# Optimization experiments

Measured on AMD Instinct MI355X. Metric: run time of the kernel, lower is better.

Reference implementation:

```python
import jax, jax.numpy as jnp
import numpy as np

# Hard-coded model hyperparams (RuntimeParams)
B, L, H, NH, FF, DEPTH = 256, 256, 128, 8, 512, 4
PEAK, NCAT, CVOC, KMAX, NNUM, NDIM, TSLOT = 500000, 8, 50001, 8, 4, 32, 256
SCALE = (H // NH) ** -0.5


def _ln(x, g, b):
    m = x.mean(-1, keepdims=True)
    v = ((x - m) ** 2).mean(-1, keepdims=True)
    return (x - m) / jnp.sqrt(v + 1e-5) * g + b


def _block(x, mask, p):
    ln1_g, ln1_b, qw, qb, ow, ob, w1, b1, w2, b2, ln2_g, ln2_b = p
    b, n, c = x.shape
    src = _ln(x, ln1_g, ln1_b)
    qkv = (src @ qw + qb).reshape(b, n, 3, NH, c // NH).transpose(2, 0, 3, 1, 4)
    q, k, v = qkv[0], qkv[1], qkv[2]  # [b, nh, n, dh]
    dots = jnp.einsum('bhid,bhjd->bhij', q, k) * SCALE
    dots = jnp.where(mask[:, None, None, :], dots, -jnp.inf)
    attn = jax.nn.softmax(dots, axis=-1)
    out = jnp.einsum('bhij,bhjd->bhid', attn, v).transpose(0, 2, 1, 3).reshape(b, n, c)
    x = x + out @ ow + ob
    h = _ln(x, ln2_g, ln2_b)
    h = jax.nn.gelu(h @ w1 + b1, approximate=False) @ w2 + b2
    return x + h


def _encode(cat_vals, cat_lens, num_arr, cat_tables, num_W):
    # Vectorized form of the per-sample _encode_fields python loop:
    # per categorical field: mean of embeddings over the ragged value list
    # per numeric field: bias-free linear projection; then mean over all fields.
    emb = cat_tables[jnp.arange(NCAT)[None, :, None], cat_vals]  # [B,F,K,H]
    pos = (jnp.arange(KMAX)[None, None, :] < cat_lens[:, :, None]).astype(emb.dtype)
    fc = (emb * pos[..., None]).sum(2) / cat_lens[:, :, None].astype(emb.dtype)  # [B,F,H]
    fn = jnp.einsum('bfd,fdh->bfh', num_arr, num_W)  # [B,Fn,H]
    return (fc.sum(1) + fn.sum(1)) / (NCAT + NNUM)  # mean over all fields


def setup_inputs() -> dict:
    key = jax.random.key(0)
    ks = iter(jax.random.split(key, 40))
    nk = lambda: next(ks)
    d = {}
    d['item_seq'] = jax.random.randint(nk(), (B, L), 0, PEAK + 5)
    d['action_seq'] = jax.random.randint(nk(), (B, L), 0, 5)
    d['time_diff'] = jax.random.randint(nk(), (B, L), 0, TSLOT)
    seq_lens = jax.random.randint(nk(), (B,), L // 2, L + 1)
    d['mask'] = jnp.arange(L)[None, :] < seq_lens[:, None]
    for pre in ('u', 'i'):
        vals = jax.random.randint(nk(), (B, NCAT, KMAX), 1, CVOC)
        lens = jax.random.randint(nk(), (B, NCAT), 1, KMAX + 1)
        vals = jnp.where(jnp.arange(KMAX)[None, None, :] < lens[:, :, None], vals, 0)
        d[pre + '_cat_vals'] = vals
        d[pre + '_cat_lens'] = lens
        d[pre + '_num'] = jax.random.normal(nk(), (B, NNUM, NDIM), dtype=jnp.float32)
    s = 0.02
    d['item_table'] = (jax.random.normal(nk(), (PEAK + 5, H), dtype=jnp.float32) * s).at[0].set(0.0)
    d['act_table'] = jax.random.normal(nk(), (5, H), dtype=jnp.float32) * s
    d['time_table'] = jax.random.normal(nk(), (TSLOT, H), dtype=jnp.float32) * s
    d['cat_tables'] = (jax.random.normal(nk(), (NCAT, CVOC, H), dtype=jnp.float32) * s).at[:, 0, :].set(0.0)
    d['num_W'] = jax.random.normal(nk(), (NNUM, NDIM, H), dtype=jnp.float32) * s
    d['global_token'] = jax.random.normal(nk(), (1, 1, H), dtype=jnp.float32)
    d['ln1_g'] = jnp.ones((DEPTH, H)); d['ln1_b'] = jnp.zeros((DEPTH, H))
    d['qkv_w'] = jax.random.normal(nk(), (DEPTH, H, 3 * H), dtype=jnp.float32) * s
    d['qkv_b'] = jnp.zeros((DEPTH, 3 * H))
    d['out_w'] = jax.random.normal(nk(), (DEPTH, H, H), dtype=jnp.float32) * s
    d['out_b'] = jnp.zeros((DEPTH, H))
    d['mlp_w1'] = jax.random.normal(nk(), (DEPTH, H, FF), dtype=jnp.float32) * s
    d['mlp_b1'] = jnp.zeros((DEPTH, FF))
    d['mlp_w2'] = jax.random.normal(nk(), (DEPTH, FF, H), dtype=jnp.float32) * s
    d['mlp_b2'] = jnp.zeros((DEPTH, H))
    d['ln2_g'] = jnp.ones((DEPTH, H)); d['ln2_b'] = jnp.zeros((DEPTH, H))
    d['bott_w'] = jax.random.normal(nk(), (H, H), dtype=jnp.float32) * s
    d['bott_b'] = jnp.zeros((H,))
    d['cls_w'] = jax.random.normal(nk(), (H, 1), dtype=jnp.float32) * s
    d['cls_b'] = jnp.zeros((1,))
    return d


def reference(item_seq, action_seq, time_diff, mask, u_cat_vals, u_cat_lens, u_num,
              i_cat_vals, i_cat_lens, i_num, item_table, act_table, time_table,
              cat_tables, num_W, global_token, ln1_g, ln1_b, qkv_w, qkv_b,
              out_w, out_b, mlp_w1, mlp_b1, mlp_w2, mlp_b2, ln2_g, ln2_b,
              bott_w, bott_b, cls_w, cls_b):
    b = item_seq.shape[0]
    seq_feat = item_table[item_seq] + act_table[action_seq] + time_table[time_diff]  # [B,L,H]
    u = _encode(u_cat_vals, u_cat_lens, u_num, cat_tables, num_W)[:, None, :]
    i = _encode(i_cat_vals, i_cat_lens, i_num, cat_tables, num_W)[:, None, :]
    cls = jnp.broadcast_to(global_token, (b, 1, H))
    x = jnp.concatenate([cls, u, i, seq_feat], axis=1)  # [B, 3+L, H]
    fmask = jnp.concatenate([jnp.ones((b, 3), dtype=bool), mask], axis=1)
    for dd in range(DEPTH):
        p = (ln1_g[dd], ln1_b[dd], qkv_w[dd], qkv_b[dd], out_w[dd], out_b[dd],
             mlp_w1[dd], mlp_b1[dd], mlp_w2[dd], mlp_b2[dd], ln2_g[dd], ln2_b[dd])
        x = _block(x, fmask, p)
    latent = x[:, 0, :]
    logits = (jax.nn.relu(latent @ bott_w + bott_b) @ cls_w + cls_b)[:, 0]
    embed = latent / jnp.maximum(jnp.linalg.norm(latent, axis=-1, keepdims=True), 1e-12)
    return logits, embed
```

## Files before the change

### kernel.cpp

```cpp
#include <hip/hip_runtime.h>
#include <cstdio>

#define BATCH 256
#define SEQL 256
#define NPOS 259
#define TTOK (BATCH*NPOS)
#define HD 128
#define NHEAD 8
#define FF 512
#define DEPTH 4
#define CVOC 50001

typedef unsigned short u16;
typedef unsigned int u32;
typedef __bf16 bf16x8 __attribute__((ext_vector_type(8)));
typedef float f32x4 __attribute__((ext_vector_type(4)));
typedef float f32x16 __attribute__((ext_vector_type(16)));

typedef const __attribute__((address_space(1))) u32 gas_u32;
typedef __attribute__((address_space(3))) u32 las_u32;
#define GLOAD16(gptr, lptr) \
  __builtin_amdgcn_global_load_lds((gas_u32*)(gptr), (las_u32*)(lptr), 16, 0, 0)

__device__ __forceinline__ u16 f2bf(float f) {
  u32 i = __float_as_uint(f);
  u32 r = (i + 0x7FFFu + ((i >> 16) & 1u)) >> 16;
  return (u16)r;
}

__global__ void k_transpose(const float* __restrict__ in, u16* __restrict__ out,
                            int D, int K, int N) {
  int idx = blockIdx.x * 256 + threadIdx.x;
  int total = D * K * N;
  if (idx >= total) return;
  int k = idx % K; int rem = idx / K; int n = rem % N; int d = rem / N;
  out[idx] = f2bf(in[(d * K + k) * N + n]);
}

__global__ __launch_bounds__(128)
void k_build(const int* __restrict__ item_seq, const int* __restrict__ act_seq,
             const int* __restrict__ tdiff,
             const int* __restrict__ ucv, const int* __restrict__ ucl, const float* __restrict__ unum,
             const int* __restrict__ icv, const int* __restrict__ icl, const float* __restrict__ inum,
             const float* __restrict__ item_t, const float* __restrict__ act_t,
             const float* __restrict__ time_t, const float* __restrict__ cat_t,
             const float* __restrict__ numW, const float* __restrict__ gtok,
             float* __restrict__ x) {
  int pos = blockIdx.x, b = blockIdx.y, h = threadIdx.x;
  float v;
  if (pos == 0) {
    v = gtok[h];
  } else if (pos <= 2) {
    const int* cv = (pos == 1) ? ucv : icv;
    const int* cl = (pos == 1) ? ucl : icl;
    const float* nm = (pos == 1) ? unum : inum;
    float acc = 0.f;
    for (int f = 0; f < 8; ++f) {
      float s = 0.f;
      for (int k = 0; k < 8; ++k) {
        int idx = cv[(b * 8 + f) * 8 + k];
        s += cat_t[((size_t)f * CVOC + idx) * HD + h];
      }
      acc += s / (float)cl[b * 8 + f];
    }
    for (int f = 0; f < 4; ++f)
      for (int d = 0; d < 32; ++d)
        acc += nm[(b * 4 + f) * 32 + d] * numW[(f * 32 + d) * HD + h];
    v = acc * (1.f / 12.f);
  } else {
    int l = pos - 3;
    v = item_t[(size_t)item_seq[b * SEQL + l] * HD + h]
      + act_t[(size_t)act_seq[b * SEQL + l] * HD + h]
      + time_t[(size_t)tdiff[b * SEQL + l] * HD + h];
  }
  x[((size_t)b * NPOS + pos) * HD + h] = v;
}

__global__ __launch_bounds__(256)
void k_ln(const float* __restrict__ x, const float* __restrict__ g,
          const float* __restrict__ be, u16* __restrict__ out) {
  int t = blockIdx.x * 4 + (threadIdx.x >> 6);
  int lane = threadIdx.x & 63;
  const float* xr = x + (size_t)t * HD;
  float a = xr[lane], c = xr[lane + 64];
  float s = a + c, s2 = a * a + c * c;
  #pragma unroll
  for (int o = 32; o; o >>= 1) { s += __shfl_xor(s, o); s2 += __shfl_xor(s2, o); }
  float mean = s * (1.f / HD);
  float var = s2 * (1.f / HD) - mean * mean;
  float rstd = rsqrtf(var + 1e-5f);
  out[(size_t)t * HD + lane]      = f2bf((a - mean) * rstd * g[lane] + be[lane]);
  out[(size_t)t * HD + lane + 64] = f2bf((c - mean) * rstd * g[lane + 64] + be[lane + 64]);
}

template <int ACT, bool QS>
__global__ __launch_bounds__(256)
void k_gemm(const u16* __restrict__ X, const u16* __restrict__ WT,
            const float* __restrict__ bias, u16* __restrict__ outp,
            int K, int N) {
  __shared__ __align__(16) u16 lA[128 * 32];
  __shared__ __align__(16) u16 lB[128 * 32];
  const int tid = threadIdx.x;
  const int wave = tid >> 6, lane = tid & 63;
  const int row0 = blockIdx.x * 128;
  const int n0 = blockIdx.y * 128;
  const int wr = (wave >> 1) * 64, wc = (wave & 1) * 64;
  const int sr = lane >> 2;
  const int sc = ((lane & 3) ^ ((lane >> 3) & 3)) << 3;
  const u16* gA0 = X  + (size_t)(row0 + wave * 16 + sr) * K + sc;
  const u16* gA1 = X  + (size_t)(row0 + 64 + wave * 16 + sr) * K + sc;
  const u16* gB0 = WT + (size_t)(n0 + wave * 16 + sr) * K + sc;
  const u16* gB1 = WT + (size_t)(n0 + 64 + wave * 16 + sr) * K + sc;
  u16* lA0 = &lA[wave * 512];
  u16* lA1 = &lA[2048 + wave * 512];
  u16* lB0 = &lB[wave * 512];
  u16* lB1 = &lB[2048 + wave * 512];
  const int q = lane & 15;
  const int cg = lane >> 4;
  const int rdoff = ((cg ^ ((q >> 1) & 3)) << 3);
  f32x4 acc[4][4] = {};
  for (int k0 = 0; k0 < K; k0 += 32) {
    __syncthreads();
    GLOAD16(gA0 + k0, lA0);
    GLOAD16(gA1 + k0, lA1);
    GLOAD16(gB0 + k0, lB0);
    GLOAD16(gB1 + k0, lB1);
    __syncthreads();
    bf16x8 af[4], bf[4];
    #pragma unroll
    for (int i = 0; i < 4; ++i)
      af[i] = *(const bf16x8*)&lA[(wr + i * 16 + q) * 32 + rdoff];
    #pragma unroll
    for (int j = 0; j < 4; ++j)
      bf[j] = *(const bf16x8*)&lB[(wc + j * 16 + q) * 32 + rdoff];
    #pragma unroll
    for (int i = 0; i < 4; ++i)
      #pragma unroll
      for (int j = 0; j < 4; ++j)
        acc[i][j] = __builtin_amdgcn_mfma_f32_16x16x32_bf16(af[i], bf[j], acc[i][j], 0, 0, 0);
  }
  const int rg4 = cg * 4;
  #pragma unroll
  for (int i = 0; i < 4; ++i) {
    #pragma unroll
    for (int j = 0; j < 4; ++j) {
      int col = n0 + wc + j * 16 + q;
      float bv = bias[col];
      float scl = (QS && col < 128) ? 0.25f : 1.f;
      #pragma unroll
      for (int jj = 0; jj < 4; ++jj) {
        int row = row0 + wr + i * 16 + rg4 + jj;
        float v = acc[i][j][jj] + bv;
        if (ACT == 1) v = 0.5f * v * (1.f + erff(v * 0.70710678118654752f));
        if (QS) v *= scl;
        outp[(size_t)row * N + col] = f2bf(v);
      }
    }
  }
}

__global__ __launch_bounds__(256)
void k_gemm_ln(const u16* __restrict__ X, const u16* __restrict__ WT,
               const float* __restrict__ bias, float* __restrict__ xio,
               const float* __restrict__ g, const float* __restrict__ be,
               u16* __restrict__ srcout, int K) {
  __shared__ __align__(16) u16 lA[128 * 32];
  __shared__ __align__(16) u16 lB[128 * 32];
  __shared__ float part[128][2][2];
  const int tid = threadIdx.x;
  const int wave = tid >> 6, lane = tid & 63;
  const int row0 = blockIdx.x * 128;
  const int wr = (wave >> 1) * 64, wc = (wave & 1) * 64;
  const int whalf = wave & 1;
  const int sr = lane >> 2;
  const int sc = ((lane & 3) ^ ((lane >> 3) & 3)) << 3;
  const u16* gA0 = X  + (size_t)(row0 + wave * 16 + sr) * K + sc;
  const u16* gA1 = X  + (size_t)(row0 + 64 + wave * 16 + sr) * K + sc;
  const u16* gB0 = WT + (size_t)(wave * 16 + sr) * K + sc;
  const u16* gB1 = WT + (size_t)(64 + wave * 16 + sr) * K + sc;
  u16* lA0 = &lA[wave * 512];
  u16* lA1 = &lA[2048 + wave * 512];
  u16* lB0 = &lB[wave * 512];
  u16* lB1 = &lB[2048 + wave * 512];
  const int q = lane & 15;
  const int cg = lane >> 4;
  const int rdoff = ((cg ^ ((q >> 1) & 3)) << 3);
  f32x4 acc[4][4] = {};
  for (int k0 = 0; k0 < K; k0 += 32) {
    __syncthreads();
    GLOAD16(gA0 + k0, lA0);
    GLOAD16(gA1 + k0, lA1);
    GLOAD16(gB0 + k0, lB0);
    GLOAD16(gB1 + k0, lB1);
    __syncthreads();
    bf16x8 af[4], bf[4];
    #pragma unroll
    for (int i = 0; i < 4; ++i)
      af[i] = *(const bf16x8*)&lA[(wr + i * 16 + q) * 32 + rdoff];
    #pragma unroll
    for (int j = 0; j < 4; ++j)
      bf[j] = *(const bf16x8*)&lB[(wc + j * 16 + q) * 32 + rdoff];
    #pragma unroll
    for (int i = 0; i < 4; ++i)
      #pragma unroll
      for (int j = 0; j < 4; ++j)
        acc[i][j] = __builtin_amdgcn_mfma_f32_16x16x32_bf16(af[i], bf[j], acc[i][j], 0, 0, 0);
  }
  const int rg4 = cg * 4;
  float ps[4][4], ps2[4][4];
  #pragma unroll
  for (int i = 0; i < 4; ++i)
    #pragma unroll
    for (int jj = 0; jj < 4; ++jj) { ps[i][jj] = 0.f; ps2[i][jj] = 0.f; }
  #pragma unroll
  for (int i = 0; i < 4; ++i) {
    #pragma unroll
    for (int j = 0; j < 4; ++j) {
      int col = wc + j * 16 + q;
      float bv = bias[col];
      #pragma unroll
      for (int jj = 0; jj < 4; ++jj) {
        int row = row0 + wr + i * 16 + rg4 + jj;
        float xv = xio[(size_t)row * 128 + col] + acc[i][j][jj] + bv;
        acc[i][j][jj] = xv;
        ps[i][jj] += xv;
        ps2[i][jj] += xv * xv;
      }
    }
  }
  #pragma unroll
  for (int o = 1; o < 16; o <<= 1) {
    #pragma unroll
    for (int i = 0; i < 4; ++i)
      #pragma unroll
      for (int jj = 0; jj < 4; ++jj) {
        ps[i][jj]  += __shfl_xor(ps[i][jj], o);
        ps2[i][jj] += __shfl_xor(ps2[i][jj], o);
      }
  }
  if (q == 0) {
    #pragma unroll
    for (int i = 0; i < 4; ++i)
      #pragma unroll
      for (int jj = 0; jj < 4; ++jj) {
        int rl = wr + i * 16 + rg4 + jj;
        part[rl][whalf][0] = ps[i][jj];
        part[rl][whalf][1] = ps2[i][jj];
      }
  }
  __syncthreads();
  #pragma unroll
  for (int i = 0; i < 4; ++i) {
    #pragma unroll
    for (int jj = 0; jj < 4; ++jj) {
      int rl = wr + i * 16 + rg4 + jj;
      float S  = part[rl][0][0] + part[rl][1][0];
      float S2 = part[rl][0][1] + part[rl][1][1];
      float mean = S * (1.f / 128.f);
      float rstd = rsqrtf(S2 * (1.f / 128.f) - mean * mean + 1e-5f);
      int row = row0 + rl;
      #pragma unroll
      for (int j = 0; j < 4; ++j) {
        int col = wc + j * 16 + q;
        float xv = acc[i][j][jj];
        xio[(size_t)row * 128 + col] = xv;
        srcout[(size_t)row * 128 + col] = f2bf((xv - mean) * rstd * g[col] + be[col]);
      }
    }
  }
}

#define VSTR2 296
__global__ __launch_bounds__(256)
void k_attn(const u16* __restrict__ qkv, const int* __restrict__ mask,
            u16* __restrict__ out) {
  int h = blockIdx.x, b = blockIdx.y;
  __shared__ __align__(16) u16 Klin[9 * 512];
  __shared__ __align__(16) u16 Vt[16 * VSTR2];
  __shared__ int part[4];
  const int tid = threadIdx.x;
  int mv = (mask[b * SEQL + tid] != 0) ? 1 : 0;
  #pragma unroll
  for (int o = 32; o; o >>= 1) mv += __shfl_xor(mv, o);
  if ((tid & 63) == 0) part[tid >> 6] = mv;
  for (int idx = tid; idx < 576; idx += 256) {
    int r = idx >> 1, h2 = idx & 1;
    uint4 val = make_uint4(0, 0, 0, 0);
    if (r < NPOS)
      val = *(const uint4*)&qkv[((size_t)(b * NPOS + r)) * 384 + h * 16 + 128 + h2 * 8];
    *(uint4*)&Klin[(r >> 5) * 512 + h2 * 256 + (r & 31) * 8] = val;
  }
  for (int r = tid; r < 288; r += 256) {
    u16 tmp[16];
    if (r < NPOS) {
      const u16* vp = &qkv[((size_t)(b * NPOS + r)) * 384 + h * 16 + 256];
      *(uint4*)&tmp[0] = *(const uint4*)&vp[0];
      *(uint4*)&tmp[8] = *(const uint4*)&vp[8];
    } else {
      #pragma unroll
      for (int d = 0; d < 16; ++d) tmp[d] = 0;
    }
    #pragma unroll
    for (int d = 0; d < 16; ++d) Vt[d * VSTR2 + r] = tmp[d];
  }
  __syncthreads();
  const int nvalid = part[0] + part[1] + part[2] + part[3] + 3;
  const int ktiles = (nvalid + 31) >> 5;
  const int wave = tid >> 6, lane = tid & 63;
  const int q5 = lane & 31, hi = lane >> 5;
  const f32x16 zf = {};
  for (int qt = wave; qt < 9; qt += 4) {
    int qrow = qt * 32 + q5;
    int qr = (qrow < NPOS) ? qrow : (NPOS - 1);
    bf16x8 qf = *(const bf16x8*)&qkv[((size_t)(b * NPOS + qr)) * 384 + h * 16 + hi * 8];
    float m = -1e30f, l = 0.f;
    f32x16 acc = {};
    for (int kt = 0; kt < ktiles; ++kt) {
      bf16x8 kf = *(const bf16x8*)&Klin[kt * 512 + lane * 8];
      f32x16 s4 = __builtin_amdgcn_mfma_f32_32x32x16_bf16(kf, qf, zf, 0, 0, 0);
      float p[16];
      float tmax = -1e30f;
      #pragma unroll
      for (int r = 0; r < 16; ++r) {
        int kr = kt * 32 + (r & 3) + 8 * (r >> 2) + 4 * hi;
        float v = (kr < nvalid) ? s4[r] : -1e30f;
        p[r] = v;
        tmax = fmaxf(tmax, v);
      }
      tmax = fmaxf(tmax, __shfl_xor(tmax, 32));
      float mnew = fmaxf(m, tmax);
      float fac = __expf(m - mnew);
      float tsum = 0.f;
      #pragma unroll
      for (int r = 0; r < 16; ++r) { p[r] = __expf(p[r] - mnew); tsum += p[r]; }
      tsum += __shfl_xor(tsum, 32);
      l = l * fac + tsum;
      m = mnew;
      #pragma unroll
      for (int r = 0; r < 8; ++r) acc[r] *= fac;
      u32 w[8], xw[8];
      #pragma unroll
      for (int i = 0; i < 8; ++i)
        asm("v_cvt_pk_bf16_f32 %0, %1, %2" : "=v"(w[i]) : "v"(p[2 * i]), "v"(p[2 * i + 1]));
      #pragma unroll
      for (int i = 0; i < 8; ++i) xw[i] = (u32)__shfl_xor((int)w[i], 32);
      union { u32 u[4]; bf16x8 v; } f1, f2;
      if (hi) {
        f1.u[0] = xw[2]; f1.u[1] = xw[3]; f1.u[2] = w[2]; f1.u[3] = w[3];
        f2.u[0] = xw[6]; f2.u[1] = xw[7]; f2.u[2] = w[6]; f2.u[3] = w[7];
      } else {
        f1.u[0] = w[0]; f1.u[1] = w[1]; f1.u[2] = xw[0]; f1.u[3] = xw[1];
        f2.u[0] = w[4]; f2.u[1] = w[5]; f2.u[2] = xw[4]; f2.u[3] = xw[5];
      }
      bf16x8 vf0 = {}, vf1 = {};
      if (q5 < 16) {
        vf0 = *(const bf16x8*)&Vt[q5 * VSTR2 + kt * 32 + hi * 8];
        vf1 = *(const bf16x8*)&Vt[q5 * VSTR2 + kt * 32 + 16 + hi * 8];
      }
      acc = __builtin_amdgcn_mfma_f32_32x32x16_bf16(vf0, f1.v, acc, 0, 0, 0);
      acc = __builtin_amdgcn_mfma_f32_32x32x16_bf16(vf1, f2.v, acc, 0, 0, 0);
    }
    if (qrow < NPOS) {
      float linv = 1.f / l;
      u16* op = &out[((size_t)(b * NPOS + qrow)) * HD + h * 16];
      u32 w0 = (u32)f2bf(acc[0] * linv) | ((u32)f2bf(acc[1] * linv) << 16);
      u32 w1 = (u32)f2bf(acc[2] * linv) | ((u32)f2bf(acc[3] * linv) << 16);
      u32 w2 = (u32)f2bf(acc[4] * linv) | ((u32)f2bf(acc[5] * linv) << 16);
      u32 w3 = (u32)f2bf(acc[6] * linv) | ((u32)f2bf(acc[7] * linv) << 16);
      *(uint2*)&op[4 * hi] = make_uint2(w0, w1);
      *(uint2*)&op[8 + 4 * hi] = make_uint2(w2, w3);
    }
  }
}

__global__ __launch_bounds__(128)
void k_head(const float* __restrict__ x, const float* __restrict__ bw,
            const float* __restrict__ bb, const float* __restrict__ cw,
             const float* __restrict__ cb, float* __restrict__ dout) {
  int b = blockIdx.x, n = threadIdx.x;
  __shared__ float lat[HD];
  __shared__ float redp[2], redss[2];
  float lv = x[((size_t)b * NPOS) * HD + n];
  lat[n] = lv;
  __syncthreads();
  float t = 0.f;
  for (int k = 0; k < HD; ++k) t += lat[k] * bw[k * HD + n];
  t += bb[n];
  t = fmaxf(t, 0.f);
  float p = t * cw[n];
  float ss = lv * lv;
  #pragma unroll
  for (int o = 32; o; o >>= 1) { p += __shfl_xor(p, o); ss += __shfl_xor(ss, o); }
  if ((n & 63) == 0) { redp[n >> 6] = p; redss[n >> 6] = ss; }
  __syncthreads();
  float psum = redp[0] + redp[1];
  float ssum = redss[0] + redss[1];
  if (n == 0) dout[b] = psum + cb[0];
  float nrm = fmaxf(sqrtf(ssum), 1e-12f);
  dout[256 + (size_t)b * HD + n] = lv / nrm;
}

extern "C" void kernel_launch(void* const* d_in, const int* in_sizes, int n_in,
                              void* d_out, int out_size, void* d_ws, size_t ws_size,
                              hipStream_t stream) {
  const int* item_seq = (const int*)d_in[0];
  const int* action_seq = (const int*)d_in[1];
  const int* time_diff = (const int*)d_in[2];
  const int* mask = (const int*)d_in[3];
  const int* u_cv = (const int*)d_in[4];
  const int* u_cl = (const int*)d_in[5];
  const float* u_num = (const float*)d_in[6];
  const int* i_cv = (const int*)d_in[7];
  const int* i_cl = (const int*)d_in[8];
  const float* i_num = (const float*)d_in[9];
  const float* item_t = (const float*)d_in[10];
  const float* act_t = (const float*)d_in[11];
  const float* time_t = (const float*)d_in[12];
  const float* cat_t = (const float*)d_in[13];
  const float* num_W = (const float*)d_in[14];
  const float* gtok = (const float*)d_in[15];
  const float* ln1_g = (const float*)d_in[16];
  const float* ln1_b = (const float*)d_in[17];
  const float* qkv_w = (const float*)d_in[18];
  const float* qkv_b = (const float*)d_in[19];
  const float* out_w = (const float*)d_in[20];
  const float* out_b = (const float*)d_in[21];
  const float* w1 = (const float*)d_in[22];
  const float* b1 = (const float*)d_in[23];
  const float* w2 = (const float*)d_in[24];
  const float* b2 = (const float*)d_in[25];
  const float* ln2_g = (const float*)d_in[26];
  const float* ln2_b = (const float*)d_in[27];
  const float* bott_w = (const float*)d_in[28];
  const float* bott_b = (const float*)d_in[29];
  const float* cls_w = (const float*)d_in[30];
  const float* cls_b = (const float*)d_in[31];

  const size_t off_x   = 0;
  const size_t off_src = 33947648;
  const size_t off_big = 50921472;
  const size_t off_wT  = 118816768;
  const size_t need    = 120389632;
  if (ws_size < need) {
    fprintf(stderr, "kernel_launch: ws_size %zu < needed %zu\n", ws_size, need);
    return;
  }
  char* ws = (char*)d_ws;
  float* x   = (float*)(ws + off_x);
  u16* src   = (u16*)(ws + off_src);
  u16* big   = (u16*)(ws + off_big);
  u16* wT    = (u16*)(ws + off_wT);
  u16* qkvT  = wT;
  u16* outT  = wT + 196608;
  u16* w1T   = wT + 262144;
  u16* w2T   = wT + 524288;

  k_transpose<<<(4 * 128 * 384 + 255) / 256, 256, 0, stream>>>(qkv_w, qkvT, 4, 128, 384);
  k_transpose<<<(4 * 128 * 128 + 255) / 256, 256, 0, stream>>>(out_w, outT, 4, 128, 128);
  k_transpose<<<(4 * 128 * 512 + 255) / 256, 256, 0, stream>>>(w1, w1T, 4, 128, 512);
  k_transpose<<<(4 * 512 * 128 + 255) / 256, 256, 0, stream>>>(w2, w2T, 4, 512, 128);

  k_build<<<dim3(NPOS, BATCH), 128, 0, stream>>>(
      item_seq, action_seq, time_diff, u_cv, u_cl, u_num, i_cv, i_cl, i_num,
      item_t, act_t, time_t, cat_t, num_W, gtok, x);

  k_ln<<<TTOK / 4, 256, 0, stream>>>(x, ln1_g, ln1_b, src);

  const int rt = TTOK / 128;
  for (int dd = 0; dd < DEPTH; ++dd) {
    k_gemm<0, true><<<dim3(rt, 3), 256, 0, stream>>>(
        src, qkvT + dd * 49152, qkv_b + dd * 384, big, 128, 384);
    k_attn<<<dim3(NHEAD, BATCH), 256, 0, stream>>>(big, mask, src);
    k_gemm_ln<<<dim3(rt, 1), 256, 0, stream>>>(
        src, outT + dd * 16384, out_b + dd * HD, x,
        ln2_g + dd * HD, ln2_b + dd * HD, src, 128);
    k_gemm<1, false><<<dim3(rt, 4), 256, 0, stream>>>(
        src, w1T + dd * 65536, b1 + dd * FF, big, 128, 512);
    const float* ng = (dd < 3) ? (ln1_g + (dd + 1) * HD) : (ln1_g + dd * HD);
    const float* nb = (dd < 3) ? (ln1_b + (dd + 1) * HD) : (ln1_b + dd * HD);
    k_gemm_ln<<<dim3(rt, 1), 256, 0, stream>>>(
        big, w2T + dd * 65536, b2 + dd * HD, x, ng, nb, src, 512);
  }

  k_head<<<BATCH, 128, 0, stream>>>(x, bott_w, bott_b, cls_w, cls_b, (float*)d_out);
}
```

Before: 840.9 us.

## Fuse weight transposes and initial LN, widen attention blocks to one wave per query tile

Merges the four weight-transpose launches into one kernel and folds the first LayerNorm into the embedding build kernel, so fewer launches run and the x buffer is not re-read. The attention kernel now runs 576 threads, nine waves with one 32-row query tile each, instead of four waves looping over tiles. It also uses exp2 with the log2e factor folded into the Q scale, and raises wave priority around the MFMA calls. Larger blocks may lower occupancy or raise register pressure in the attention kernel.

```diff
diff --git a/kernel.cpp b/kernel.cpp
--- a/kernel.cpp
+++ b/kernel.cpp
@@ -22,19 +22,26 @@
 #define GLOAD16(gptr, lptr) \
   __builtin_amdgcn_global_load_lds((gas_u32*)(gptr), (las_u32*)(lptr), 16, 0, 0)
 
+#define QSCALE 0.36067376022224085f
+
 __device__ __forceinline__ u16 f2bf(float f) {
   u32 i = __float_as_uint(f);
   u32 r = (i + 0x7FFFu + ((i >> 16) & 1u)) >> 16;
   return (u16)r;
 }
 
-__global__ void k_transpose(const float* __restrict__ in, u16* __restrict__ out,
-                            int D, int K, int N) {
+__global__ void k_transpose_all(const float* __restrict__ qkv_w, const float* __restrict__ out_w,
+                                const float* __restrict__ w1, const float* __restrict__ w2,
+                                u16* __restrict__ wT) {
   int idx = blockIdx.x * 256 + threadIdx.x;
-  int total = D * K * N;
-  if (idx >= total) return;
-  int k = idx % K; int rem = idx / K; int n = rem % N; int d = rem / N;
-  out[idx] = f2bf(in[(d * K + k) * N + n]);
+  const float* in; int K, N, local;
+  if (idx < 196608)      { in = qkv_w; K = 128; N = 384; local = idx; }
+  else if (idx < 262144) { in = out_w; K = 128; N = 128; local = idx - 196608; }
+  else if (idx < 524288) { in = w1;    K = 128; N = 512; local = idx - 262144; }
+  else if (idx < 786432) { in = w2;    K = 512; N = 128; local = idx - 524288; }
+  else return;
+  int k = local % K; int rem = local / K; int n = rem % N; int d = rem / N;
+  wT[idx] = f2bf(in[(d * K + k) * N + n]);
 }
 
 __global__ __launch_bounds__(128)
@@ -45,7 +52,8 @@
              const float* __restrict__ item_t, const float* __restrict__ act_t,
              const float* __restrict__ time_t, const float* __restrict__ cat_t,
              const float* __restrict__ numW, const float* __restrict__ gtok,
-             float* __restrict__ x) {
+             const float* __restrict__ g, const float* __restrict__ be,
+             float* __restrict__ x, u16* __restrict__ src) {
   int pos = blockIdx.x, b = blockIdx.y, h = threadIdx.x;
   float v;
   if (pos == 0) {
@@ -73,24 +81,18 @@
       + act_t[(size_t)act_seq[b * SEQL + l] * HD + h]
       + time_t[(size_t)tdiff[b * SEQL + l] * HD + h];
   }
-  x[((size_t)b * NPOS + pos) * HD + h] = v;
-}
-
-__global__ __launch_bounds__(256)
-void k_ln(const float* __restrict__ x, const float* __restrict__ g,
-          const float* __restrict__ be, u16* __restrict__ out) {
-  int t = blockIdx.x * 4 + (threadIdx.x >> 6);
-  int lane = threadIdx.x & 63;
-  const float* xr = x + (size_t)t * HD;
-  float a = xr[lane], c = xr[lane + 64];
-  float s = a + c, s2 = a * a + c * c;
+  size_t t = (size_t)b * NPOS + pos;
+  x[t * HD + h] = v;
+  __shared__ float red[2][2];
+  float s = v, s2 = v * v;
   #pragma unroll
   for (int o = 32; o; o >>= 1) { s += __shfl_xor(s, o); s2 += __shfl_xor(s2, o); }
-  float mean = s * (1.f / HD);
-  float var = s2 * (1.f / HD) - mean * mean;
-  float rstd = rsqrtf(var + 1e-5f);
-  out[(size_t)t * HD + lane]      = f2bf((a - mean) * rstd * g[lane] + be[lane]);
-  out[(size_t)t * HD + lane + 64] = f2bf((c - mean) * rstd * g[lane + 64] + be[lane + 64]);
+  if ((h & 63) == 0) { red[h >> 6][0] = s; red[h >> 6][1] = s2; }
+  __syncthreads();
+  float S = red[0][0] + red[1][0], S2 = red[0][1] + red[1][1];
+  float mean = S * (1.f / HD);
+  float rstd = rsqrtf(S2 * (1.f / HD) - mean * mean + 1e-5f);
+  src[t * HD + h] = f2bf((v - mean) * rstd * g[h] + be[h]);
 }
 
 template <int ACT, bool QS>
@@ -146,7 +148,7 @@
     for (int j = 0; j < 4; ++j) {
       int col = n0 + wc + j * 16 + q;
       float bv = bias[col];
-      float scl = (QS && col < 128) ? 0.25f : 1.f;
+      float scl = (QS && col < 128) ? QSCALE : 1.f;
       #pragma unroll
       for (int jj = 0; jj < 4; ++jj) {
         int row = row0 + wr + i * 16 + rg4 + jj;
@@ -271,7 +273,7 @@
 }
 
 #define VSTR2 296
-__global__ __launch_bounds__(256)
+__global__ __launch_bounds__(576)
 void k_attn(const u16* __restrict__ qkv, const int* __restrict__ mask,
             u16* __restrict__ out) {
   int h = blockIdx.x, b = blockIdx.y;
@@ -279,18 +281,21 @@
   __shared__ __align__(16) u16 Vt[16 * VSTR2];
   __shared__ int part[4];
   const int tid = threadIdx.x;
-  int mv = (mask[b * SEQL + tid] != 0) ? 1 : 0;
-  #pragma unroll
-  for (int o = 32; o; o >>= 1) mv += __shfl_xor(mv, o);
-  if ((tid & 63) == 0) part[tid >> 6] = mv;
-  for (int idx = tid; idx < 576; idx += 256) {
-    int r = idx >> 1, h2 = idx & 1;
+  if (tid < 256) {
+    int mv = (mask[b * SEQL + tid] != 0) ? 1 : 0;
+    #pragma unroll
+    for (int o = 32; o; o >>= 1) mv += __shfl_xor(mv, o);
+    if ((tid & 63) == 0) part[tid >> 6] = mv;
+  }
+  {
+    int r = tid >> 1, h2 = tid & 1;
     uint4 val = make_uint4(0, 0, 0, 0);
     if (r < NPOS)
       val = *(const uint4*)&qkv[((size_t)(b * NPOS + r)) * 384 + h * 16 + 128 + h2 * 8];
     *(uint4*)&Klin[(r >> 5) * 512 + h2 * 256 + (r & 31) * 8] = val;
   }
-  for (int r = tid; r < 288; r += 256) {
+  if (tid < 288) {
+    int r = tid;
     u16 tmp[16];
     if (r < NPOS) {
       const u16* vp = &qkv[((size_t)(b * NPOS + r)) * 384 + h * 16 + 256];
@@ -309,74 +314,77 @@
   const int wave = tid >> 6, lane = tid & 63;
   const int q5 = lane & 31, hi = lane >> 5;
   const f32x16 zf = {};
-  for (int qt = wave; qt < 9; qt += 4) {
-    int qrow = qt * 32 + q5;
-    int qr = (qrow < NPOS) ? qrow : (NPOS - 1);
-    bf16x8 qf = *(const bf16x8*)&qkv[((size_t)(b * NPOS + qr)) * 384 + h * 16 + hi * 8];
-    float m = -1e30f, l = 0.f;
-    f32x16 acc = {};
-    for (int kt = 0; kt < ktiles; ++kt) {
-      bf16x8 kf = *(const bf16x8*)&Klin[kt * 512 + lane * 8];
-      f32x16 s4 = __builtin_amdgcn_mfma_f32_32x32x16_bf16(kf, qf, zf, 0, 0, 0);
-      float p[16];
-      float tmax = -1e30f;
-      #pragma unroll
-      for (int r = 0; r < 16; ++r) {
-        int kr = kt * 32 + (r & 3) + 8 * (r >> 2) + 4 * hi;
-        float v = (kr < nvalid) ? s4[r] : -1e30f;
-        p[r] = v;
-        tmax = fmaxf(tmax, v);
-      }
-      tmax = fmaxf(tmax, __shfl_xor(tmax, 32));
-      float mnew = fmaxf(m, tmax);
-      float fac = __expf(m - mnew);
-      float tsum = 0.f;
-      #pragma unroll
-      for (int r = 0; r < 16; ++r) { p[r] = __expf(p[r] - mnew); tsum += p[r]; }
-      tsum += __shfl_xor(tsum, 32);
-      l = l * fac + tsum;
-      m = mnew;
-      #pragma unroll
-      for (int r = 0; r < 8; ++r) acc[r] *= fac;
-      u32 w[8], xw[8];
-      #pragma unroll
-      for (int i = 0; i < 8; ++i)
-        asm("v_cvt_pk_bf16_f32 %0, %1, %2" : "=v"(w[i]) : "v"(p[2 * i]), "v"(p[2 * i + 1]));
-      #pragma unroll
-      for (int i = 0; i < 8; ++i) xw[i] = (u32)__shfl_xor((int)w[i], 32);
-      union { u32 u[4]; bf16x8 v; } f1, f2;
-      if (hi) {
-        f1.u[0] = xw[2]; f1.u[1] = xw[3]; f1.u[2] = w[2]; f1.u[3] = w[3];
-        f2.u[0] = xw[6]; f2.u[1] = xw[7]; f2.u[2] = w[6]; f2.u[3] = w[7];
-      } else {
-        f1.u[0] = w[0]; f1.u[1] = w[1]; f1.u[2] = xw[0]; f1.u[3] = xw[1];
-        f2.u[0] = w[4]; f2.u[1] = w[5]; f2.u[2] = xw[4]; f2.u[3] = xw[5];
-      }
-      bf16x8 vf0 = {}, vf1 = {};
-      if (q5 < 16) {
-        vf0 = *(const bf16x8*)&Vt[q5 * VSTR2 + kt * 32 + hi * 8];
-        vf1 = *(const bf16x8*)&Vt[q5 * VSTR2 + kt * 32 + 16 + hi * 8];
-      }
-      acc = __builtin_amdgcn_mfma_f32_32x32x16_bf16(vf0, f1.v, acc, 0, 0, 0);
-      acc = __builtin_amdgcn_mfma_f32_32x32x16_bf16(vf1, f2.v, acc, 0, 0, 0);
-    }
-    if (qrow < NPOS) {
-      float linv = 1.f / l;
-      u16* op = &out[((size_t)(b * NPOS + qrow)) * HD + h * 16];
-      u32 w0 = (u32)f2bf(acc[0] * linv) | ((u32)f2bf(acc[1] * linv) << 16);
-      u32 w1 = (u32)f2bf(acc[2] * linv) | ((u32)f2bf(acc[3] * linv) << 16);
-      u32 w2 = (u32)f2bf(acc[4] * linv) | ((u32)f2bf(acc[5] * linv) << 16);
-      u32 w3 = (u32)f2bf(acc[6] * linv) | ((u32)f2bf(acc[7] * linv) << 16);
-      *(uint2*)&op[4 * hi] = make_uint2(w0, w1);
-      *(uint2*)&op[8 + 4 * hi] = make_uint2(w2, w3);
-    }
+  const int qt = wave;
+  int qrow = qt * 32 + q5;
+  int qr = (qrow < NPOS) ? qrow : (NPOS - 1);
+  bf16x8 qf = *(const bf16x8*)&qkv[((size_t)(b * NPOS + qr)) * 384 + h * 16 + hi * 8];
+  float m = -1e30f, l = 0.f;
+  f32x16 acc = {};
+  for (int kt = 0; kt < ktiles; ++kt) {
+    bf16x8 kf = *(const bf16x8*)&Klin[kt * 512 + lane * 8];
+    __builtin_amdgcn_s_setprio(1);
+    f32x16 s4 = __builtin_amdgcn_mfma_f32_32x32x16_bf16(kf, qf, zf, 0, 0, 0);
+    __builtin_amdgcn_s_setprio(0);
+    float p[16];
+    float tmax = -1e30f;
+    #pragma unroll
+    for (int r = 0; r < 16; ++r) {
+      int kr = kt * 32 + (r & 3) + 8 * (r >> 2) + 4 * hi;
+      float v = (kr < nvalid) ? s4[r] : -1e30f;
+      p[r] = v;
+      tmax = fmaxf(tmax, v);
+    }
+    tmax = fmaxf(tmax, __shfl_xor(tmax, 32));
+    float mnew = fmaxf(m, tmax);
+    float fac = exp2f(m - mnew);
+    float tsum = 0.f;
+    #pragma unroll
+    for (int r = 0; r < 16; ++r) { p[r] = exp2f(p[r] - mnew); tsum += p[r]; }
+    tsum += __shfl_xor(tsum, 32);
+    l = l * fac + tsum;
+    m = mnew;
+    #pragma unroll
+    for (int r = 0; r < 8; ++r) acc[r] *= fac;
+    u32 w[8], xw[8];
+    #pragma unroll
+    for (int i = 0; i < 8; ++i)
+      asm("v_cvt_pk_bf16_f32 %0, %1, %2" : "=v"(w[i]) : "v"(p[2 * i]), "v"(p[2 * i + 1]));
+    #pragma unroll
+    for (int i = 0; i < 8; ++i) xw[i] = (u32)__shfl_xor((int)w[i], 32);
+    union { u32 u[4]; bf16x8 v; } f1, f2;
+    if (hi) {
+      f1.u[0] = xw[2]; f1.u[1] = xw[3]; f1.u[2] = w[2]; f1.u[3] = w[3];
+      f2.u[0] = xw[6]; f2.u[1] = xw[7]; f2.u[2] = w[6]; f2.u[3] = w[7];
+    } else {
+      f1.u[0] = w[0]; f1.u[1] = w[1]; f1.u[2] = xw[0]; f1.u[3] = xw[1];
+      f2.u[0] = w[4]; f2.u[1] = w[5]; f2.u[2] = xw[4]; f2.u[3] = xw[5];
+    }
+    bf16x8 vf0 = {}, vf1 = {};
+    if (q5 < 16) {
+      vf0 = *(const bf16x8*)&Vt[q5 * VSTR2 + kt * 32 + hi * 8];
+      vf1 = *(const bf16x8*)&Vt[q5 * VSTR2 + kt * 32 + 16 + hi * 8];
+    }
+    __builtin_amdgcn_s_setprio(1);
+    acc = __builtin_amdgcn_mfma_f32_32x32x16_bf16(vf0, f1.v, acc, 0, 0, 0);
+    acc = __builtin_amdgcn_mfma_f32_32x32x16_bf16(vf1, f2.v, acc, 0, 0, 0);
+    __builtin_amdgcn_s_setprio(0);
+  }
+  if (qrow < NPOS) {
+    float linv = 1.f / l;
+    u16* op = &out[((size_t)(b * NPOS + qrow)) * HD + h * 16];
+    u32 w0 = (u32)f2bf(acc[0] * linv) | ((u32)f2bf(acc[1] * linv) << 16);
+    u32 w1 = (u32)f2bf(acc[2] * linv) | ((u32)f2bf(acc[3] * linv) << 16);
+    u32 w2 = (u32)f2bf(acc[4] * linv) | ((u32)f2bf(acc[5] * linv) << 16);
+    u32 w3 = (u32)f2bf(acc[6] * linv) | ((u32)f2bf(acc[7] * linv) << 16);
+    *(uint2*)&op[4 * hi] = make_uint2(w0, w1);
+    *(uint2*)&op[8 + 4 * hi] = make_uint2(w2, w3);
   }
 }
 
 __global__ __launch_bounds__(128)
 void k_head(const float* __restrict__ x, const float* __restrict__ bw,
             const float* __restrict__ bb, const float* __restrict__ cw,
-             const float* __restrict__ cb, float* __restrict__ dout) {
+            const float* __restrict__ cb, float* __restrict__ dout) {
   int b = blockIdx.x, n = threadIdx.x;
   __shared__ float lat[HD];
   __shared__ float redp[2], redss[2];
@@ -455,22 +463,17 @@
   u16* w1T   = wT + 262144;
   u16* w2T   = wT + 524288;
 
-  k_transpose<<<(4 * 128 * 384 + 255) / 256, 256, 0, stream>>>(qkv_w, qkvT, 4, 128, 384);
-  k_transpose<<<(4 * 128 * 128 + 255) / 256, 256, 0, stream>>>(out_w, outT, 4, 128, 128);
-  k_transpose<<<(4 * 128 * 512 + 255) / 256, 256, 0, stream>>>(w1, w1T, 4, 128, 512);
-  k_transpose<<<(4 * 512 * 128 + 255) / 256, 256, 0, stream>>>(w2, w2T, 4, 512, 128);
+  k_transpose_all<<<3072, 256, 0, stream>>>(qkv_w, out_w, w1, w2, wT);
 
   k_build<<<dim3(NPOS, BATCH), 128, 0, stream>>>(
       item_seq, action_seq, time_diff, u_cv, u_cl, u_num, i_cv, i_cl, i_num,
-      item_t, act_t, time_t, cat_t, num_W, gtok, x);
-
-  k_ln<<<TTOK / 4, 256, 0, stream>>>(x, ln1_g, ln1_b, src);
+      item_t, act_t, time_t, cat_t, num_W, gtok, ln1_g, ln1_b, x, src);
 
   const int rt = TTOK / 128;
   for (int dd = 0; dd < DEPTH; ++dd) {
     k_gemm<0, true><<<dim3(rt, 3), 256, 0, stream>>>(
         src, qkvT + dd * 49152, qkv_b + dd * 384, big, 128, 384);
-    k_attn<<<dim3(NHEAD, BATCH), 256, 0, stream>>>(big, mask, src);
+    k_attn<<<dim3(NHEAD, BATCH), 576, 0, stream>>>(big, mask, src);
     k_gemm_ln<<<dim3(rt, 1), 256, 0, stream>>>(
         src, outT + dd * 16384, out_b + dd * HD, x,
         ln2_g + dd * HD, ln2_b + dd * HD, src, 128);
```

New measurement: 806.8 us. 4.1% less time.
